# Kernel tuning notes

Hardware: AMD Instinct MI355X
Metric: run time of the kernel (lower is better)

Reference implementation:

```python
import jax, jax.numpy as jnp
import numpy as np

H = 12          # num_heads
T = 8           # num_temp_tokens (frames per video clip)


def _conv1d(z, w, b):
    # z: (Bv, C, T), w: (C_out, C_in, 3), padding=1, stride=1 (matches nn.Conv1d)
    y = jax.lax.conv_general_dilated(z, w, window_strides=(1,), padding=[(1, 1)],
                                     dimension_numbers=('NCH', 'OIH', 'NCH'))
    return y + b[None, :, None]


def setup_inputs() -> dict:
    key = jax.random.key(0)
    ks = jax.random.split(key, 9)
    B, N, C = 64, 197, 768
    s = 0.02
    return {
        'x': jax.random.normal(ks[0], (B, N, C), jnp.float32),
        'w_qkv': jax.random.normal(ks[1], (3 * C, C), jnp.float32) * s,
        'b_qkv': jax.random.normal(ks[2], (3 * C,), jnp.float32) * s,
        'w_proj': jax.random.normal(ks[3], (C, C), jnp.float32) * s,
        'b_proj': jax.random.normal(ks[4], (C,), jnp.float32) * s,
        'conv_q_w': jax.random.normal(ks[5], (C, C, 3), jnp.float32) * s,
        'conv_q_b': jax.random.normal(ks[6], (C,), jnp.float32) * s,
        'conv_k_w': jax.random.normal(ks[7], (C, C, 3), jnp.float32) * s,
        'conv_k_b': jax.random.normal(ks[8], (C,), jnp.float32) * s,
    }


def reference(x, w_qkv, b_qkv, w_proj, b_proj, conv_q_w, conv_q_b, conv_k_w, conv_k_b):
    B, N, C = x.shape
    Dh = C // H
    scale = Dh ** -0.5

    # temporal context from the CLS token across frames of each clip
    g = x[:, 0, :].reshape(B // T, T, C).transpose(0, 2, 1)          # (Bv, C, T)
    tcq = _conv1d(g, conv_q_w, conv_q_b).transpose(0, 2, 1).reshape(B, H, 1, Dh)
    tck = _conv1d(g, conv_k_w, conv_k_b).transpose(0, 2, 1).reshape(B, H, 1, Dh)

    qkv = (x @ w_qkv.T + b_qkv).reshape(B, N, 3, H, Dh).transpose(2, 0, 3, 1, 4)
    q, k, v = qkv[0], qkv[1], qkv[2]                                  # (B, H, N, Dh)

    # bias-added attention: (q + tcq) (k + tck)^T
    scores = jnp.einsum('bhnd,bhmd->bhnm', q + tcq, k + tck) * scale  # (B, H, N, N)
    attn = jax.nn.softmax(scores, axis=-1)
    out = jnp.einsum('bhnm,bhmd->bhnd', attn, v)                      # (B, H, N, Dh)
    out = out.transpose(0, 2, 1, 3).reshape(B, N, C)
    return out @ w_proj.T + b_proj
```

## Files before the change

kernel.cpp:

```cpp
#include <hip/hip_runtime.h>
#include <hip/hip_bf16.h>
#include <stdint.h>

typedef __attribute__((ext_vector_type(8))) short s16x8;
typedef __attribute__((ext_vector_type(4))) float f32x4;

#define MFMA16(a, b, c) __builtin_amdgcn_mfma_f32_16x16x32_bf16((a), (b), (c), 0, 0, 0)
#define SBAR() __builtin_amdgcn_s_barrier()

__device__ __forceinline__ void gl_lds16(const void* g, void* l) {
  __builtin_amdgcn_global_load_lds(
      (__attribute__((address_space(1))) void*)(void*)g,
      (__attribute__((address_space(3))) void*)l,
      16, 0, 0);
}

__device__ __forceinline__ unsigned short f2bf(float f) {
  union { float f; uint32_t u; } c; c.f = f;
  return (unsigned short)((c.u + 0x7FFFu + ((c.u >> 16) & 1u)) >> 16);
}

__device__ __forceinline__ f32x4 max4(f32x4 a, f32x4 b) {
  f32x4 c;
  c[0] = fmaxf(a[0], b[0]); c[1] = fmaxf(a[1], b[1]);
  c[2] = fmaxf(a[2], b[2]); c[3] = fmaxf(a[3], b[3]);
  return c;
}

__device__ __forceinline__ void xcd_swz(int GX, int GY, int& bx, int& by) {
  int nwg = GX * GY;
  int lid = by * GX + bx;
  int q = nwg >> 3, rm = nwg & 7;
  int xcd = lid & 7, off = lid >> 3;
  int nid = (xcd < rm ? xcd * (q + 1) : rm * (q + 1) + (xcd - rm) * q) + off;
  bx = nid % GX;
  by = nid / GX;
}

__global__ __launch_bounds__(256) void cvt_conv(
    const float* __restrict__ x, unsigned short* __restrict__ x_bf, int na4,
    const float* __restrict__ wqkv, unsigned short* __restrict__ wqkv_bf, int nb4,
    const float* __restrict__ wproj, unsigned short* __restrict__ wproj_bf, int nc4,
    const float* __restrict__ cqw, const float* __restrict__ ckw,
    float* __restrict__ tcpq, float* __restrict__ tcpk) {
  const int tid = threadIdx.x;
  const int bid = blockIdx.x;
  if (bid < 768) {
    __shared__ float g[192][10];
    const int clip = bid / 96;
    const int rem = bid % 96;
    const int chunk = rem >> 2;
    const int part = rem & 3;
    const int ci0 = part * 192;
    for (int i = tid; i < 192 * 8; i += 256) {
      int tt = i / 192, ci = i % 192;
      g[ci][tt + 1] = x[(size_t)(clip * 8 + tt) * 151296 + ci0 + ci];
    }
    for (int i = tid; i < 192; i += 256) { g[i][0] = 0.f; g[i][9] = 0.f; }
    __syncthreads();
    const int co = chunk * 32 + (tid >> 3);
    const int t = tid & 7;
    float aq = 0.f, ak = 0.f;
    const float* wqp = cqw + (size_t)co * 2304 + ci0 * 3;
    const float* wkp = ckw + (size_t)co * 2304 + ci0 * 3;
    for (int ci = 0; ci < 192; ++ci) {
      float g0 = g[ci][t], g1 = g[ci][t + 1], g2 = g[ci][t + 2];
      aq += g0 * wqp[ci * 3 + 0] + g1 * wqp[ci * 3 + 1] + g2 * wqp[ci * 3 + 2];
      ak += g0 * wkp[ci * 3 + 0] + g1 * wkp[ci * 3 + 1] + g2 * wkp[ci * 3 + 2];
    }
    int b = clip * 8 + t;
    tcpq[part * 49152 + b * 768 + co] = aq;
    tcpk[part * 49152 + b * 768 + co] = ak;
    return;
  }
  int i = (bid - 768) * 256 + tid;
  const float* src; unsigned short* dst; int j;
  if (i < na4) { src = x; dst = x_bf; j = i; }
  else if (i < na4 + nb4) { src = wqkv; dst = wqkv_bf; j = i - na4; }
  else if (i < na4 + nb4 + nc4) { src = wproj; dst = wproj_bf; j = i - na4 - nb4; }
  else return;
  float4 v = ((const float4*)src)[j];
  ushort4 o;
  o.x = f2bf(v.x); o.y = f2bf(v.y); o.z = f2bf(v.z); o.w = f2bf(v.w);
  ((ushort4*)dst)[j] = o;
}

__global__ __launch_bounds__(1024, 4) void qkv_attn(
    const unsigned short* __restrict__ X,
    const unsigned short* __restrict__ Wq,
    const float* __restrict__ bias,
    const float* __restrict__ tcpq, const float* __restrict__ tcpk,
    unsigned short* __restrict__ O) {
  union __align__(16) Smem {
    struct {
      unsigned short Xs[3][208][64];
      unsigned short Ws[3][192][64];
    } st;
    struct {
      unsigned short Qs[208][72];
      unsigned short Ks[208][72];
      unsigned short VTs[64][232];
      unsigned short Ps[13][16][40];
    } at;
  };
  __shared__ Smem U;
  __shared__ float tcb[3][64];

  const int tid = threadIdx.x;
  const int w = tid >> 6, lane = tid & 63;
  int bx = blockIdx.x, by0 = 0;
  xcd_swz(gridDim.x, 1, bx, by0);
  const int b = bx / 12, h = bx % 12;

  if (tid < 192) {
    int sec = tid >> 6, d = tid & 63;
    float v = bias[sec * 768 + h * 64 + d];
    if (sec < 2) {
      const float* tp = (sec == 0) ? tcpq : tcpk;
      int idx = b * 768 + h * 64 + d;
#pragma unroll
      for (int p = 0; p < 4; ++p) v += tp[p * 49152 + idx];
    }
    tcb[sec][d] = v;
  }

  const int wm = w >> 2, wn = w & 3;
  const int r = lane & 15, gq = lane >> 4;
  const int lrow = lane >> 3;
  const int lsw = ((lane & 7) ^ (lrow & 7)) * 8;
  const int mfn = (wm == 3) ? 4 : 3;

  f32x4 acc[4][3] = {};
  const size_t xbase = (size_t)b * 197 * 768;

  const int swzk[2] = { ((0 + gq) ^ (r & 7)) * 16, ((4 + gq) ^ (r & 7)) * 16 };
  const int rowA = (wm * 48 + r) * 128;
  const int rowB = (wn * 48 + r) * 128;

  auto stage = [&](int buf, int kc) {
#pragma unroll
    for (int j = 0; j < 2; ++j) {
      int c = w + j * 16;
      if (c < 26) {
        int row = c * 8 + lrow;
        gl_lds16(X + xbase + (size_t)row * 768 + kc * 64 + lsw,
                 (char*)&U.st.Xs[buf][0][0] + c * 1024);
      }
    }
#pragma unroll
    for (int j = 0; j < 2; ++j) {
      int c = w + j * 16;
      if (c < 24) {
        int wrow = c * 8 + lrow;
        int sec = wrow >> 6;
        gl_lds16(Wq + (size_t)(sec * 768 + h * 64 + (wrow & 63)) * 768 + kc * 64 + lsw,
                 (char*)&U.st.Ws[buf][0][0] + c * 1024);
      }
    }
  };

#define WAIT_OWN()                                                 \
  do {                                                             \
    if (w < 8)       asm volatile("s_waitcnt vmcnt(4)" ::: "memory"); \
    else if (w < 10) asm volatile("s_waitcnt vmcnt(3)" ::: "memory"); \
    else             asm volatile("s_waitcnt vmcnt(2)" ::: "memory"); \
  } while (0)

  stage(0, 0);
  stage(1, 1);
  WAIT_OWN();
  SBAR();

#pragma unroll
  for (int kc = 0; kc < 12; ++kc) {
    if (kc + 2 < 12) stage((kc + 2) % 3, kc + 2);
    const char* xb = (const char*)&U.st.Xs[kc % 3][0][0] + rowA;
    const char* wb = (const char*)&U.st.Ws[kc % 3][0][0] + rowB;
    __builtin_amdgcn_s_setprio(1);
#pragma unroll
    for (int kk = 0; kk < 2; ++kk) {
      s16x8 bfrg[3];
#pragma unroll
      for (int nf = 0; nf < 3; ++nf)
        bfrg[nf] = *(const s16x8*)(wb + nf * 2048 + swzk[kk]);
#pragma unroll
      for (int mf = 0; mf < 4; ++mf) {
        if (mf < mfn) {
          s16x8 afr = *(const s16x8*)(xb + mf * 2048 + swzk[kk]);
#pragma unroll
          for (int nf = 0; nf < 3; ++nf) acc[mf][nf] = MFMA16(afr, bfrg[nf], acc[mf][nf]);
        }
      }
    }
    __builtin_amdgcn_s_setprio(0);
    if (kc < 10) {
      WAIT_OWN();
      SBAR();
    } else if (kc == 10) {
      asm volatile("s_waitcnt vmcnt(0)" ::: "memory");
      SBAR();
    }
  }
  __syncthreads();

  for (int i = tid; i < 64 * 35; i += 1024) {
    int d = i / 35, c = 197 + i % 35;
    U.at.VTs[d][c] = 0;
  }
#pragma unroll
  for (int mf = 0; mf < 4; ++mf) {
    if (mf < mfn) {
#pragma unroll
      for (int nf = 0; nf < 3; ++nf) {
        int ncol = wn * 48 + nf * 16 + r;
        int sec = ncol >> 6, d = ncol & 63;
        float bb = tcb[sec][d];
#pragma unroll
        for (int rr = 0; rr < 4; ++rr) {
          int mrow = wm * 48 + mf * 16 + gq * 4 + rr;
          unsigned short bv = f2bf(acc[mf][nf][rr] + bb);
          if (sec == 0)      U.at.Qs[mrow][d] = bv;
          else if (sec == 1) U.at.Ks[mrow][d] = bv;
          else if (mrow < 197) U.at.VTs[d][mrow] = bv;
        }
      }
    }
  }
  __syncthreads();

  const int g = gq;
  for (int qt = w; qt < 13; qt += 16) {
    const int q0 = qt * 16;
    int qrow = q0 + r; if (qrow > 196) qrow = 196;
    s16x8 aq0 = *(const s16x8*)&U.at.Qs[qrow][g * 8];
    s16x8 aq1 = *(const s16x8*)&U.at.Qs[qrow][32 + g * 8];

    f32x4 s[13];
    __builtin_amdgcn_s_setprio(1);
#pragma unroll
    for (int j = 0; j < 13; ++j) {
      f32x4 z = {};
      z = MFMA16(aq0, *(const s16x8*)&U.at.Ks[j * 16 + r][g * 8], z);
      z = MFMA16(aq1, *(const s16x8*)&U.at.Ks[j * 16 + r][32 + g * 8], z);
      s[j] = z;
    }
    __builtin_amdgcn_s_setprio(0);
    if (r >= 5) { s[12][0] = -1e30f; s[12][1] = -1e30f; s[12][2] = -1e30f; s[12][3] = -1e30f; }

    f32x4 mx = s[0];
#pragma unroll
    for (int j = 1; j < 13; ++j) mx = max4(mx, s[j]);
#pragma unroll
    for (int off = 1; off < 16; off <<= 1) {
      f32x4 o_;
      o_[0] = __shfl_xor(mx[0], off, 64); o_[1] = __shfl_xor(mx[1], off, 64);
      o_[2] = __shfl_xor(mx[2], off, 64); o_[3] = __shfl_xor(mx[3], off, 64);
      mx = max4(mx, o_);
    }
    const float cexp = 0.125f * 1.44269504088896f;
    f32x4 sum = {};
#pragma unroll
    for (int j = 0; j < 13; ++j) {
      f32x4 p;
      p[0] = exp2f((s[j][0] - mx[0]) * cexp); p[1] = exp2f((s[j][1] - mx[1]) * cexp);
      p[2] = exp2f((s[j][2] - mx[2]) * cexp); p[3] = exp2f((s[j][3] - mx[3]) * cexp);
      s[j] = p;
      sum += p;
    }
#pragma unroll
    for (int off = 1; off < 16; off <<= 1) {
      sum[0] += __shfl_xor(sum[0], off, 64); sum[1] += __shfl_xor(sum[1], off, 64);
      sum[2] += __shfl_xor(sum[2], off, 64); sum[3] += __shfl_xor(sum[3], off, 64);
    }

    f32x4 o4[4] = {};
    for (int ks = 0; ks < 7; ++ks) {
      int j0 = ks * 2;
#pragma unroll
      for (int jj = 0; jj < 2; ++jj) {
        int jt = j0 + jj;
        int colb = jj * 16 + r;
        if (jt < 13) {
          f32x4 p = s[jt < 13 ? jt : 0];
          U.at.Ps[w][g * 4 + 0][colb] = f2bf(p[0]);
          U.at.Ps[w][g * 4 + 1][colb] = f2bf(p[1]);
          U.at.Ps[w][g * 4 + 2][colb] = f2bf(p[2]);
          U.at.Ps[w][g * 4 + 3][colb] = f2bf(p[3]);
        } else {
          U.at.Ps[w][g * 4 + 0][colb] = 0; U.at.Ps[w][g * 4 + 1][colb] = 0;
          U.at.Ps[w][g * 4 + 2][colb] = 0; U.at.Ps[w][g * 4 + 3][colb] = 0;
        }
      }
      asm volatile("s_waitcnt lgkmcnt(0)" ::: "memory");
      s16x8 ap = *(const s16x8*)&U.at.Ps[w][r][g * 8];
      __builtin_amdgcn_s_setprio(1);
#pragma unroll
      for (int n = 0; n < 4; ++n)
        o4[n] = MFMA16(ap, *(const s16x8*)&U.at.VTs[n * 16 + r][ks * 32 + g * 8], o4[n]);
      __builtin_amdgcn_s_setprio(0);
    }

    f32x4 rinv;
    rinv[0] = 1.0f / sum[0]; rinv[1] = 1.0f / sum[1];
    rinv[2] = 1.0f / sum[2]; rinv[3] = 1.0f / sum[3];
#pragma unroll
    for (int n = 0; n < 4; ++n) {
#pragma unroll
      for (int rr = 0; rr < 4; ++rr) {
        int qr = q0 + g * 4 + rr;
        if (qr < 197)
          O[((size_t)(b * 197 + qr)) * 768 + h * 64 + n * 16 + r] = f2bf(o4[n][rr] * rinv[rr]);
      }
    }
  }
#undef WAIT_OWN
}

__global__ __launch_bounds__(1024, 4) void proj_gemm(
    const unsigned short* __restrict__ A,
    const unsigned short* __restrict__ Bw,
    const float* __restrict__ bias,
    float* __restrict__ Out) {
  __shared__ __align__(16) unsigned short Xs[3][208][64];
  __shared__ __align__(16) unsigned short Ws[3][192][64];
  const int tid = threadIdx.x;
  const int w = tid >> 6, lane = tid & 63;
  int bx = blockIdx.x, by0 = 0;
  xcd_swz(gridDim.x, 1, bx, by0);
  const int b = bx >> 2, nt = bx & 3;
  const int wm = w >> 2, wn = w & 3;
  const int r = lane & 15, gq = lane >> 4;
  const int lrow = lane >> 3;
  const int lsw = ((lane & 7) ^ (lrow & 7)) * 8;
  const int mfn = (wm == 3) ? 4 : 3;

  f32x4 acc[4][3] = {};
  const size_t abase = (size_t)b * 197 * 768;
  const int swzk[2] = { ((0 + gq) ^ (r & 7)) * 16, ((4 + gq) ^ (r & 7)) * 16 };
  const int rowA = (wm * 48 + r) * 128;
  const int rowB = (wn * 48 + r) * 128;

  auto stage = [&](int buf, int kc) {
#pragma unroll
    for (int j = 0; j < 2; ++j) {
      int c = w + j * 16;
      if (c < 26) {
        int row = c * 8 + lrow;
        gl_lds16(A + abase + (size_t)row * 768 + kc * 64 + lsw,
                 (char*)&Xs[buf][0][0] + c * 1024);
      }
    }
#pragma unroll
    for (int j = 0; j < 2; ++j) {
      int c = w + j * 16;
      if (c < 24) {
        int wrow = c * 8 + lrow;
        gl_lds16(Bw + (size_t)(nt * 192 + wrow) * 768 + kc * 64 + lsw,
                 (char*)&Ws[buf][0][0] + c * 1024);
      }
    }
  };

#define WAIT_OWN()                                                 \
  do {                                                             \
    if (w < 8)       asm volatile("s_waitcnt vmcnt(4)" ::: "memory"); \
    else if (w < 10) asm volatile("s_waitcnt vmcnt(3)" ::: "memory"); \
    else             asm volatile("s_waitcnt vmcnt(2)" ::: "memory"); \
  } while (0)

  stage(0, 0);
  stage(1, 1);
  WAIT_OWN();
  SBAR();

#pragma unroll
  for (int kc = 0; kc < 12; ++kc) {
    if (kc + 2 < 12) stage((kc + 2) % 3, kc + 2);
    const char* xb = (const char*)&Xs[kc % 3][0][0] + rowA;
    const char* wb = (const char*)&Ws[kc % 3][0][0] + rowB;
    __builtin_amdgcn_s_setprio(1);
#pragma unroll
    for (int kk = 0; kk < 2; ++kk) {
      s16x8 bfrg[3];
#pragma unroll
      for (int nf = 0; nf < 3; ++nf)
        bfrg[nf] = *(const s16x8*)(wb + nf * 2048 + swzk[kk]);
#pragma unroll
      for (int mf = 0; mf < 4; ++mf) {
        if (mf < mfn) {
          s16x8 afr = *(const s16x8*)(xb + mf * 2048 + swzk[kk]);
#pragma unroll
          for (int nf = 0; nf < 3; ++nf) acc[mf][nf] = MFMA16(afr, bfrg[nf], acc[mf][nf]);
        }
      }
    }
    __builtin_amdgcn_s_setprio(0);
    if (kc < 10) {
      WAIT_OWN();
      SBAR();
    } else if (kc == 10) {
      asm volatile("s_waitcnt vmcnt(0)" ::: "memory");
      SBAR();
    }
  }

#pragma unroll
  for (int mf = 0; mf < 4; ++mf) {
    if (mf < mfn) {
#pragma unroll
      for (int nf = 0; nf < 3; ++nf) {
        int N = nt * 192 + wn * 48 + nf * 16 + r;
        float bb = bias[N];
#pragma unroll
        for (int rr = 0; rr < 4; ++rr) {
          int mrow = wm * 48 + mf * 16 + gq * 4 + rr;
          if (mrow < 197)
            Out[((size_t)(b * 197 + mrow)) * 768 + N] = acc[mf][nf][rr] + bb;
        }
      }
    }
  }
#undef WAIT_OWN
}

extern "C" void kernel_launch(void* const* d_in, const int* in_sizes, int n_in,
                              void* d_out, int out_size, void* d_ws, size_t ws_size,
                              hipStream_t stream) {
  const float* x       = (const float*)d_in[0];
  const float* w_qkv   = (const float*)d_in[1];
  const float* b_qkv   = (const float*)d_in[2];
  const float* w_proj  = (const float*)d_in[3];
  const float* b_proj  = (const float*)d_in[4];
  const float* conv_qw = (const float*)d_in[5];
  const float* conv_qb = (const float*)d_in[6];
  const float* conv_kw = (const float*)d_in[7];
  const float* conv_kb = (const float*)d_in[8];
  float* out = (float*)d_out;

  char* ws = (char*)d_ws;
  size_t off = 0;
  auto alloc = [&](size_t n) {
    char* p = ws + off;
    off = (off + n + 255) & ~(size_t)255;
    return p;
  };
  unsigned short* x_bf    = (unsigned short*)alloc(12608ull * 768 * 2);
  unsigned short* ao_bf   = (unsigned short*)alloc(12608ull * 768 * 2);
  unsigned short* wqkv_bf = (unsigned short*)alloc(2304ull * 768 * 2);
  unsigned short* wproj_bf= (unsigned short*)alloc(768ull * 768 * 2);
  float* tcpq = (float*)alloc(4ull * 64 * 768 * 4);
  float* tcpk = (float*)alloc(4ull * 64 * 768 * 4);
  if (off > ws_size) return;

  float* bias_comb = (float*)alloc(2304ull * 4);
  {
  }

  const int na4 = 2420736, nb4 = 442368, nc4 = 147456;
  const int cvt_blocks = (na4 + nb4 + nc4 + 255) / 256;
  cvt_conv<<<dim3(768 + cvt_blocks), 256, 0, stream>>>(
      x, x_bf, na4, w_qkv, wqkv_bf, nb4, w_proj, wproj_bf, nc4,
      conv_qw, conv_kw, tcpq, tcpk);
  {
    struct L {
      static __global__ void k(const float* bq, const float* cq, const float* ck,
                               float* o) {
        int i = blockIdx.x * 256 + threadIdx.x;
        if (i >= 2304) return;
        float v = bq[i];
        if (i < 768) v += cq[i];
        else if (i < 1536) v += ck[i - 768];
        o[i] = v;
      }
    };
    L::k<<<dim3(9), 256, 0, stream>>>(b_qkv, conv_qb, conv_kb, bias_comb);
  }
  qkv_attn<<<dim3(768), 1024, 0, stream>>>(x_bf, wqkv_bf, bias_comb, tcpq, tcpk, ao_bf);
  proj_gemm<<<dim3(256), 1024, 0, stream>>>(ao_bf, wproj_bf, b_proj, out);
}
```

Baseline: 152.7 us.

## Warp-specialize GEMM mainloops into producer and consumer waves; fold bias kernel into cvt

Both the fused QKV+attention kernel and the projection GEMM now use warp specialization. Waves 8-15 only issue global-to-LDS loads, and waves 0-7 only run MFMAs, each covering 112 rows × 48 columns with larger accumulator tiles. This aims to separate memory issue from compute and cut per-wave wait overhead, at the cost of half the waves doing no math and more accumulator registers per compute wave. The small bias-combining kernel is merged into the conversion kernel as one extra block, which saves a launch.

Result: slower. 285.5 us (+87.0%).

```diff
diff --git a/kernel.cpp b/kernel.cpp
--- a/kernel.cpp
+++ b/kernel.cpp
@@ -42,7 +42,9 @@
     const float* __restrict__ wqkv, unsigned short* __restrict__ wqkv_bf, int nb4,
     const float* __restrict__ wproj, unsigned short* __restrict__ wproj_bf, int nc4,
     const float* __restrict__ cqw, const float* __restrict__ ckw,
-    float* __restrict__ tcpq, float* __restrict__ tcpk) {
+    float* __restrict__ tcpq, float* __restrict__ tcpk,
+    const float* __restrict__ bqkv, const float* __restrict__ cqb,
+    const float* __restrict__ ckb, float* __restrict__ bias_comb, int last_bid) {
   const int tid = threadIdx.x;
   const int bid = blockIdx.x;
   if (bid < 768) {
@@ -71,6 +73,15 @@
     int b = clip * 8 + t;
     tcpq[part * 49152 + b * 768 + co] = aq;
     tcpk[part * 49152 + b * 768 + co] = ak;
+    return;
+  }
+  if (bid == last_bid) {
+    for (int i = tid; i < 2304; i += 256) {
+      float v = bqkv[i];
+      if (i < 768) v += cqb[i];
+      else if (i < 1536) v += ckb[i - 768];
+      bias_comb[i] = v;
+    }
     return;
   }
   int i = (bid - 768) * 256 + tid;
@@ -124,23 +135,24 @@
     tcb[sec][d] = v;
   }
 
-  const int wm = w >> 2, wn = w & 3;
   const int r = lane & 15, gq = lane >> 4;
   const int lrow = lane >> 3;
   const int lsw = ((lane & 7) ^ (lrow & 7)) * 8;
-  const int mfn = (wm == 3) ? 4 : 3;
-
-  f32x4 acc[4][3] = {};
+
+  const int wm = (w >> 2) & 1, wn = w & 3;
+  const int mfn = (wm == 0) ? 7 : 6;
+  const int swzk[2] = { ((0 + gq) ^ (r & 7)) * 16, ((4 + gq) ^ (r & 7)) * 16 };
+  const int rowA = (wm * 112 + r) * 128;
+  const int rowB = (wn * 48 + r) * 128;
+
+  f32x4 acc[7][3] = {};
   const size_t xbase = (size_t)b * 197 * 768;
 
-  const int swzk[2] = { ((0 + gq) ^ (r & 7)) * 16, ((4 + gq) ^ (r & 7)) * 16 };
-  const int rowA = (wm * 48 + r) * 128;
-  const int rowB = (wn * 48 + r) * 128;
-
+  const int pw = w - 8;
   auto stage = [&](int buf, int kc) {
 #pragma unroll
-    for (int j = 0; j < 2; ++j) {
-      int c = w + j * 16;
+    for (int j = 0; j < 4; ++j) {
+      int c = pw + j * 8;
       if (c < 26) {
         int row = c * 8 + lrow;
         gl_lds16(X + xbase + (size_t)row * 768 + kc * 64 + lsw,
@@ -148,58 +160,56 @@
       }
     }
 #pragma unroll
-    for (int j = 0; j < 2; ++j) {
-      int c = w + j * 16;
-      if (c < 24) {
-        int wrow = c * 8 + lrow;
-        int sec = wrow >> 6;
-        gl_lds16(Wq + (size_t)(sec * 768 + h * 64 + (wrow & 63)) * 768 + kc * 64 + lsw,
-                 (char*)&U.st.Ws[buf][0][0] + c * 1024);
-      }
+    for (int j = 0; j < 3; ++j) {
+      int c = pw + j * 8;
+      int wrow = c * 8 + lrow;
+      int sec = wrow >> 6;
+      gl_lds16(Wq + (size_t)(sec * 768 + h * 64 + (wrow & 63)) * 768 + kc * 64 + lsw,
+               (char*)&U.st.Ws[buf][0][0] + c * 1024);
     }
   };
 
-#define WAIT_OWN()                                                 \
-  do {                                                             \
-    if (w < 8)       asm volatile("s_waitcnt vmcnt(4)" ::: "memory"); \
-    else if (w < 10) asm volatile("s_waitcnt vmcnt(3)" ::: "memory"); \
-    else             asm volatile("s_waitcnt vmcnt(2)" ::: "memory"); \
+#define WAIT_P()                                                      \
+  do {                                                                \
+    if (w < 10) asm volatile("s_waitcnt vmcnt(7)" ::: "memory");      \
+    else        asm volatile("s_waitcnt vmcnt(6)" ::: "memory");      \
   } while (0)
 
-  stage(0, 0);
-  stage(1, 1);
-  WAIT_OWN();
+  if (w >= 8) {
+    stage(0, 0);
+    stage(1, 1);
+    WAIT_P();
+  }
   SBAR();
 
 #pragma unroll
   for (int kc = 0; kc < 12; ++kc) {
-    if (kc + 2 < 12) stage((kc + 2) % 3, kc + 2);
-    const char* xb = (const char*)&U.st.Xs[kc % 3][0][0] + rowA;
-    const char* wb = (const char*)&U.st.Ws[kc % 3][0][0] + rowB;
-    __builtin_amdgcn_s_setprio(1);
-#pragma unroll
-    for (int kk = 0; kk < 2; ++kk) {
-      s16x8 bfrg[3];
-#pragma unroll
-      for (int nf = 0; nf < 3; ++nf)
-        bfrg[nf] = *(const s16x8*)(wb + nf * 2048 + swzk[kk]);
-#pragma unroll
-      for (int mf = 0; mf < 4; ++mf) {
-        if (mf < mfn) {
-          s16x8 afr = *(const s16x8*)(xb + mf * 2048 + swzk[kk]);
-#pragma unroll
-          for (int nf = 0; nf < 3; ++nf) acc[mf][nf] = MFMA16(afr, bfrg[nf], acc[mf][nf]);
+    if (w >= 8) {
+      if (kc + 2 < 12) stage((kc + 2) % 3, kc + 2);
+      if (kc < 10) WAIT_P();
+      else if (kc == 10) asm volatile("s_waitcnt vmcnt(0)" ::: "memory");
+    } else {
+      const char* xb = (const char*)&U.st.Xs[kc % 3][0][0] + rowA;
+      const char* wb = (const char*)&U.st.Ws[kc % 3][0][0] + rowB;
+      __builtin_amdgcn_s_setprio(1);
+#pragma unroll
+      for (int kk = 0; kk < 2; ++kk) {
+        s16x8 bfrg[3];
+#pragma unroll
+        for (int nf = 0; nf < 3; ++nf)
+          bfrg[nf] = *(const s16x8*)(wb + nf * 2048 + swzk[kk]);
+#pragma unroll
+        for (int mf = 0; mf < 7; ++mf) {
+          if (mf < mfn) {
+            s16x8 afr = *(const s16x8*)(xb + mf * 2048 + swzk[kk]);
+#pragma unroll
+            for (int nf = 0; nf < 3; ++nf) acc[mf][nf] = MFMA16(afr, bfrg[nf], acc[mf][nf]);
+          }
         }
       }
-    }
-    __builtin_amdgcn_s_setprio(0);
-    if (kc < 10) {
-      WAIT_OWN();
-      SBAR();
-    } else if (kc == 10) {
-      asm volatile("s_waitcnt vmcnt(0)" ::: "memory");
-      SBAR();
-    }
+      __builtin_amdgcn_s_setprio(0);
+    }
+    SBAR();
   }
   __syncthreads();
 
@@ -207,21 +217,23 @@
     int d = i / 35, c = 197 + i % 35;
     U.at.VTs[d][c] = 0;
   }
-#pragma unroll
-  for (int mf = 0; mf < 4; ++mf) {
-    if (mf < mfn) {
-#pragma unroll
-      for (int nf = 0; nf < 3; ++nf) {
-        int ncol = wn * 48 + nf * 16 + r;
-        int sec = ncol >> 6, d = ncol & 63;
-        float bb = tcb[sec][d];
-#pragma unroll
-        for (int rr = 0; rr < 4; ++rr) {
-          int mrow = wm * 48 + mf * 16 + gq * 4 + rr;
-          unsigned short bv = f2bf(acc[mf][nf][rr] + bb);
-          if (sec == 0)      U.at.Qs[mrow][d] = bv;
-          else if (sec == 1) U.at.Ks[mrow][d] = bv;
-          else if (mrow < 197) U.at.VTs[d][mrow] = bv;
+  if (w < 8) {
+#pragma unroll
+    for (int mf = 0; mf < 7; ++mf) {
+      if (mf < mfn) {
+#pragma unroll
+        for (int nf = 0; nf < 3; ++nf) {
+          int ncol = wn * 48 + nf * 16 + r;
+          int sec = ncol >> 6, d = ncol & 63;
+          float bb = tcb[sec][d];
+#pragma unroll
+          for (int rr = 0; rr < 4; ++rr) {
+            int mrow = wm * 112 + mf * 16 + gq * 4 + rr;
+            unsigned short bv = f2bf(acc[mf][nf][rr] + bb);
+            if (sec == 0)      U.at.Qs[mrow][d] = bv;
+            else if (sec == 1) U.at.Ks[mrow][d] = bv;
+            else if (mrow < 197) U.at.VTs[d][mrow] = bv;
+          }
         }
       }
     }
@@ -313,7 +325,7 @@
       }
     }
   }
-#undef WAIT_OWN
+#undef WAIT_P
 }
 
 __global__ __launch_bounds__(1024, 4) void proj_gemm(
@@ -328,22 +340,24 @@
   int bx = blockIdx.x, by0 = 0;
   xcd_swz(gridDim.x, 1, bx, by0);
   const int b = bx >> 2, nt = bx & 3;
-  const int wm = w >> 2, wn = w & 3;
   const int r = lane & 15, gq = lane >> 4;
   const int lrow = lane >> 3;
   const int lsw = ((lane & 7) ^ (lrow & 7)) * 8;
-  const int mfn = (wm == 3) ? 4 : 3;
-
-  f32x4 acc[4][3] = {};
+
+  const int wm = (w >> 2) & 1, wn = w & 3;
+  const int mfn = (wm == 0) ? 7 : 6;
+  const int swzk[2] = { ((0 + gq) ^ (r & 7)) * 16, ((4 + gq) ^ (r & 7)) * 16 };
+  const int rowA = (wm * 112 + r) * 128;
+  const int rowB = (wn * 48 + r) * 128;
+
+  f32x4 acc[7][3] = {};
   const size_t abase = (size_t)b * 197 * 768;
-  const int swzk[2] = { ((0 + gq) ^ (r & 7)) * 16, ((4 + gq) ^ (r & 7)) * 16 };
-  const int rowA = (wm * 48 + r) * 128;
-  const int rowB = (wn * 48 + r) * 128;
+  const int pw = w - 8;
 
   auto stage = [&](int buf, int kc) {
 #pragma unroll
-    for (int j = 0; j < 2; ++j) {
-      int c = w + j * 16;
+    for (int j = 0; j < 4; ++j) {
+      int c = pw + j * 8;
       if (c < 26) {
         int row = c * 8 + lrow;
         gl_lds16(A + abase + (size_t)row * 768 + kc * 64 + lsw,
@@ -351,76 +365,76 @@
       }
     }
 #pragma unroll
-    for (int j = 0; j < 2; ++j) {
-      int c = w + j * 16;
-      if (c < 24) {
-        int wrow = c * 8 + lrow;
-        gl_lds16(Bw + (size_t)(nt * 192 + wrow) * 768 + kc * 64 + lsw,
-                 (char*)&Ws[buf][0][0] + c * 1024);
-      }
+    for (int j = 0; j < 3; ++j) {
+      int c = pw + j * 8;
+      int wrow = c * 8 + lrow;
+      gl_lds16(Bw + (size_t)(nt * 192 + wrow) * 768 + kc * 64 + lsw,
+               (char*)&Ws[buf][0][0] + c * 1024);
     }
   };
 
-#define WAIT_OWN()                                                 \
-  do {                                                             \
-    if (w < 8)       asm volatile("s_waitcnt vmcnt(4)" ::: "memory"); \
-    else if (w < 10) asm volatile("s_waitcnt vmcnt(3)" ::: "memory"); \
-    else             asm volatile("s_waitcnt vmcnt(2)" ::: "memory"); \
+#define WAIT_P()                                                      \
+  do {                                                                \
+    if (w < 10) asm volatile("s_waitcnt vmcnt(7)" ::: "memory");      \
+    else        asm volatile("s_waitcnt vmcnt(6)" ::: "memory");      \
   } while (0)
 
-  stage(0, 0);
-  stage(1, 1);
-  WAIT_OWN();
+  if (w >= 8) {
+    stage(0, 0);
+    stage(1, 1);
+    WAIT_P();
+  }
   SBAR();
 
 #pragma unroll
   for (int kc = 0; kc < 12; ++kc) {
-    if (kc + 2 < 12) stage((kc + 2) % 3, kc + 2);
-    const char* xb = (const char*)&Xs[kc % 3][0][0] + rowA;
-    const char* wb = (const char*)&Ws[kc % 3][0][0] + rowB;
-    __builtin_amdgcn_s_setprio(1);
-#pragma unroll
-    for (int kk = 0; kk < 2; ++kk) {
-      s16x8 bfrg[3];
-#pragma unroll
-      for (int nf = 0; nf < 3; ++nf)
-        bfrg[nf] = *(const s16x8*)(wb + nf * 2048 + swzk[kk]);
-#pragma unroll
-      for (int mf = 0; mf < 4; ++mf) {
-        if (mf < mfn) {
-          s16x8 afr = *(const s16x8*)(xb + mf * 2048 + swzk[kk]);
-#pragma unroll
-          for (int nf = 0; nf < 3; ++nf) acc[mf][nf] = MFMA16(afr, bfrg[nf], acc[mf][nf]);
+    if (w >= 8) {
+      if (kc + 2 < 12) stage((kc + 2) % 3, kc + 2);
+      if (kc < 10) WAIT_P();
+      else if (kc == 10) asm volatile("s_waitcnt vmcnt(0)" ::: "memory");
+    } else {
+      const char* xb = (const char*)&Xs[kc % 3][0][0] + rowA;
+      const char* wb = (const char*)&Ws[kc % 3][0][0] + rowB;
+      __builtin_amdgcn_s_setprio(1);
+#pragma unroll
+      for (int kk = 0; kk < 2; ++kk) {
+        s16x8 bfrg[3];
+#pragma unroll
+        for (int nf = 0; nf < 3; ++nf)
+          bfrg[nf] = *(const s16x8*)(wb + nf * 2048 + swzk[kk]);
+#pragma unroll
+        for (int mf = 0; mf < 7; ++mf) {
+          if (mf < mfn) {
+            s16x8 afr = *(const s16x8*)(xb + mf * 2048 + swzk[kk]);
+#pragma unroll
+            for (int nf = 0; nf < 3; ++nf) acc[mf][nf] = MFMA16(afr, bfrg[nf], acc[mf][nf]);
+          }
         }
       }
-    }
-    __builtin_amdgcn_s_setprio(0);
-    if (kc < 10) {
-      WAIT_OWN();
-      SBAR();
-    } else if (kc == 10) {
-      asm volatile("s_waitcnt vmcnt(0)" ::: "memory");
-      SBAR();
-    }
-  }
-
-#pragma unroll
-  for (int mf = 0; mf < 4; ++mf) {
-    if (mf < mfn) {
-#pragma unroll
-      for (int nf = 0; nf < 3; ++nf) {
-        int N = nt * 192 + wn * 48 + nf * 16 + r;
-        float bb = bias[N];
-#pragma unroll
-        for (int rr = 0; rr < 4; ++rr) {
-          int mrow = wm * 48 + mf * 16 + gq * 4 + rr;
-          if (mrow < 197)
-            Out[((size_t)(b * 197 + mrow)) * 768 + N] = acc[mf][nf][rr] + bb;
+      __builtin_amdgcn_s_setprio(0);
+    }
+    SBAR();
+  }
+
+  if (w < 8) {
+#pragma unroll
+    for (int mf = 0; mf < 7; ++mf) {
+      if (mf < mfn) {
+#pragma unroll
+        for (int nf = 0; nf < 3; ++nf) {
+          int N = nt * 192 + wn * 48 + nf * 16 + r;
+          float bb = bias[N];
+#pragma unroll
+          for (int rr = 0; rr < 4; ++rr) {
+            int mrow = wm * 112 + mf * 16 + gq * 4 + rr;
+            if (mrow < 197)
+              Out[((size_t)(b * 197 + mrow)) * 768 + N] = acc[mf][nf][rr] + bb;
+          }
         }
       }
     }
   }
-#undef WAIT_OWN
+#undef WAIT_P
 }
 
 extern "C" void kernel_launch(void* const* d_in, const int* in_sizes, int n_in,
@@ -450,31 +464,16 @@
   unsigned short* wproj_bf= (unsigned short*)alloc(768ull * 768 * 2);
   float* tcpq = (float*)alloc(4ull * 64 * 768 * 4);
   float* tcpk = (float*)alloc(4ull * 64 * 768 * 4);
+  float* bias_comb = (float*)alloc(2304ull * 4);
   if (off > ws_size) return;
-
-  float* bias_comb = (float*)alloc(2304ull * 4);
-  {
-  }
 
   const int na4 = 2420736, nb4 = 442368, nc4 = 147456;
   const int cvt_blocks = (na4 + nb4 + nc4 + 255) / 256;
-  cvt_conv<<<dim3(768 + cvt_blocks), 256, 0, stream>>>(
+  const int last_bid = 768 + cvt_blocks;
+  cvt_conv<<<dim3(last_bid + 1), 256, 0, stream>>>(
       x, x_bf, na4, w_qkv, wqkv_bf, nb4, w_proj, wproj_bf, nc4,
-      conv_qw, conv_kw, tcpq, tcpk);
-  {
-    struct L {
-      static __global__ void k(const float* bq, const float* cq, const float* ck,
-                               float* o) {
-        int i = blockIdx.x * 256 + threadIdx.x;
-        if (i >= 2304) return;
-        float v = bq[i];
-        if (i < 768) v += cq[i];
-        else if (i < 1536) v += ck[i - 768];
-        o[i] = v;
-      }
-    };
-    L::k<<<dim3(9), 256, 0, stream>>>(b_qkv, conv_qb, conv_kb, bias_comb);
-  }
+      conv_qw, conv_kw, tcpq, tcpk,
+      b_qkv, conv_qb, conv_kb, bias_comb, last_bid);
   qkv_attn<<<dim3(768), 1024, 0, stream>>>(x_bf, wqkv_bf, bias_comb, tcpq, tcpk, ao_bf);
   proj_gemm<<<dim3(256), 1024, 0, stream>>>(ao_bf, wproj_bf, b_proj, out);
 }
```

## Warp-specialize QKV GEMM with dedicated producer waves and fold bias kernel into conversion

Applied to the files above, without the earlier changes.

The QKV projection loop inside the fused attention kernel is restructured so 4 waves only issue global-to-LDS loads and 12 waves only run MFMAs on a reshaped 80-row M tiling. Consumers no longer wait on their own loads, only on the shared barrier, which is meant to hide load latency behind compute. The small bias-combination kernel is merged into the conversion kernel as an extra block, removing one launch. The trade-off is fewer MFMA waves doing more work each, plus higher register pressure from the 5x3 accumulator tile.

New measurement: 159.8 us. +4.7%, slower.

```diff
diff --git a/kernel.cpp b/kernel.cpp
--- a/kernel.cpp
+++ b/kernel.cpp
@@ -42,7 +42,9 @@
     const float* __restrict__ wqkv, unsigned short* __restrict__ wqkv_bf, int nb4,
     const float* __restrict__ wproj, unsigned short* __restrict__ wproj_bf, int nc4,
     const float* __restrict__ cqw, const float* __restrict__ ckw,
-    float* __restrict__ tcpq, float* __restrict__ tcpk) {
+    float* __restrict__ tcpq, float* __restrict__ tcpk,
+    const float* __restrict__ bqkv, const float* __restrict__ cqb,
+    const float* __restrict__ ckb, float* __restrict__ bias_comb, int last_bid) {
   const int tid = threadIdx.x;
   const int bid = blockIdx.x;
   if (bid < 768) {
@@ -71,6 +73,15 @@
     int b = clip * 8 + t;
     tcpq[part * 49152 + b * 768 + co] = aq;
     tcpk[part * 49152 + b * 768 + co] = ak;
+    return;
+  }
+  if (bid == last_bid) {
+    for (int i = tid; i < 2304; i += 256) {
+      float v = bqkv[i];
+      if (i < 768) v += cqb[i];
+      else if (i < 1536) v += ckb[i - 768];
+      bias_comb[i] = v;
+    }
     return;
   }
   int i = (bid - 768) * 256 + tid;
@@ -124,23 +135,24 @@
     tcb[sec][d] = v;
   }
 
-  const int wm = w >> 2, wn = w & 3;
   const int r = lane & 15, gq = lane >> 4;
   const int lrow = lane >> 3;
   const int lsw = ((lane & 7) ^ (lrow & 7)) * 8;
-  const int mfn = (wm == 3) ? 4 : 3;
-
-  f32x4 acc[4][3] = {};
+
+  const int wm = w >> 2, wn = w & 3;
+  const int mfn = (wm == 2) ? 3 : 5;
+  const int swzk[2] = { ((0 + gq) ^ (r & 7)) * 16, ((4 + gq) ^ (r & 7)) * 16 };
+  const int rowA = (wm * 80 + r) * 128;
+  const int rowB = (wn * 48 + r) * 128;
+
+  f32x4 acc[5][3] = {};
   const size_t xbase = (size_t)b * 197 * 768;
 
-  const int swzk[2] = { ((0 + gq) ^ (r & 7)) * 16, ((4 + gq) ^ (r & 7)) * 16 };
-  const int rowA = (wm * 48 + r) * 128;
-  const int rowB = (wn * 48 + r) * 128;
-
+  const int pw = w - 12;
   auto stage = [&](int buf, int kc) {
 #pragma unroll
-    for (int j = 0; j < 2; ++j) {
-      int c = w + j * 16;
+    for (int j = 0; j < 7; ++j) {
+      int c = pw + j * 4;
       if (c < 26) {
         int row = c * 8 + lrow;
         gl_lds16(X + xbase + (size_t)row * 768 + kc * 64 + lsw,
@@ -148,58 +160,56 @@
       }
     }
 #pragma unroll
-    for (int j = 0; j < 2; ++j) {
-      int c = w + j * 16;
-      if (c < 24) {
-        int wrow = c * 8 + lrow;
-        int sec = wrow >> 6;
-        gl_lds16(Wq + (size_t)(sec * 768 + h * 64 + (wrow & 63)) * 768 + kc * 64 + lsw,
-                 (char*)&U.st.Ws[buf][0][0] + c * 1024);
-      }
+    for (int j = 0; j < 6; ++j) {
+      int c = pw + j * 4;
+      int wrow = c * 8 + lrow;
+      int sec = wrow >> 6;
+      gl_lds16(Wq + (size_t)(sec * 768 + h * 64 + (wrow & 63)) * 768 + kc * 64 + lsw,
+               (char*)&U.st.Ws[buf][0][0] + c * 1024);
     }
   };
 
-#define WAIT_OWN()                                                 \
-  do {                                                             \
-    if (w < 8)       asm volatile("s_waitcnt vmcnt(4)" ::: "memory"); \
-    else if (w < 10) asm volatile("s_waitcnt vmcnt(3)" ::: "memory"); \
-    else             asm volatile("s_waitcnt vmcnt(2)" ::: "memory"); \
+#define WAIT_P()                                                      \
+  do {                                                                \
+    if (pw < 2) asm volatile("s_waitcnt vmcnt(13)" ::: "memory");     \
+    else        asm volatile("s_waitcnt vmcnt(12)" ::: "memory");     \
   } while (0)
 
-  stage(0, 0);
-  stage(1, 1);
-  WAIT_OWN();
+  if (w >= 12) {
+    stage(0, 0);
+    stage(1, 1);
+    WAIT_P();
+  }
   SBAR();
 
 #pragma unroll
   for (int kc = 0; kc < 12; ++kc) {
-    if (kc + 2 < 12) stage((kc + 2) % 3, kc + 2);
-    const char* xb = (const char*)&U.st.Xs[kc % 3][0][0] + rowA;
-    const char* wb = (const char*)&U.st.Ws[kc % 3][0][0] + rowB;
-    __builtin_amdgcn_s_setprio(1);
-#pragma unroll
-    for (int kk = 0; kk < 2; ++kk) {
-      s16x8 bfrg[3];
-#pragma unroll
-      for (int nf = 0; nf < 3; ++nf)
-        bfrg[nf] = *(const s16x8*)(wb + nf * 2048 + swzk[kk]);
-#pragma unroll
-      for (int mf = 0; mf < 4; ++mf) {
-        if (mf < mfn) {
-          s16x8 afr = *(const s16x8*)(xb + mf * 2048 + swzk[kk]);
-#pragma unroll
-          for (int nf = 0; nf < 3; ++nf) acc[mf][nf] = MFMA16(afr, bfrg[nf], acc[mf][nf]);
+    if (w >= 12) {
+      if (kc + 2 < 12) stage((kc + 2) % 3, kc + 2);
+      if (kc < 10) WAIT_P();
+      else if (kc == 10) asm volatile("s_waitcnt vmcnt(0)" ::: "memory");
+    } else {
+      const char* xb = (const char*)&U.st.Xs[kc % 3][0][0] + rowA;
+      const char* wb = (const char*)&U.st.Ws[kc % 3][0][0] + rowB;
+      __builtin_amdgcn_s_setprio(1);
+#pragma unroll
+      for (int kk = 0; kk < 2; ++kk) {
+        s16x8 bfrg[3];
+#pragma unroll
+        for (int nf = 0; nf < 3; ++nf)
+          bfrg[nf] = *(const s16x8*)(wb + nf * 2048 + swzk[kk]);
+#pragma unroll
+        for (int mf = 0; mf < 5; ++mf) {
+          if (mf < mfn) {
+            s16x8 afr = *(const s16x8*)(xb + mf * 2048 + swzk[kk]);
+#pragma unroll
+            for (int nf = 0; nf < 3; ++nf) acc[mf][nf] = MFMA16(afr, bfrg[nf], acc[mf][nf]);
+          }
         }
       }
-    }
-    __builtin_amdgcn_s_setprio(0);
-    if (kc < 10) {
-      WAIT_OWN();
-      SBAR();
-    } else if (kc == 10) {
-      asm volatile("s_waitcnt vmcnt(0)" ::: "memory");
-      SBAR();
-    }
+      __builtin_amdgcn_s_setprio(0);
+    }
+    SBAR();
   }
   __syncthreads();
 
@@ -207,21 +217,23 @@
     int d = i / 35, c = 197 + i % 35;
     U.at.VTs[d][c] = 0;
   }
-#pragma unroll
-  for (int mf = 0; mf < 4; ++mf) {
-    if (mf < mfn) {
-#pragma unroll
-      for (int nf = 0; nf < 3; ++nf) {
-        int ncol = wn * 48 + nf * 16 + r;
-        int sec = ncol >> 6, d = ncol & 63;
-        float bb = tcb[sec][d];
-#pragma unroll
-        for (int rr = 0; rr < 4; ++rr) {
-          int mrow = wm * 48 + mf * 16 + gq * 4 + rr;
-          unsigned short bv = f2bf(acc[mf][nf][rr] + bb);
-          if (sec == 0)      U.at.Qs[mrow][d] = bv;
-          else if (sec == 1) U.at.Ks[mrow][d] = bv;
-          else if (mrow < 197) U.at.VTs[d][mrow] = bv;
+  if (w < 12) {
+#pragma unroll
+    for (int mf = 0; mf < 5; ++mf) {
+      if (mf < mfn) {
+#pragma unroll
+        for (int nf = 0; nf < 3; ++nf) {
+          int ncol = wn * 48 + nf * 16 + r;
+          int sec = ncol >> 6, d = ncol & 63;
+          float bb = tcb[sec][d];
+#pragma unroll
+          for (int rr = 0; rr < 4; ++rr) {
+            int mrow = wm * 80 + mf * 16 + gq * 4 + rr;
+            unsigned short bv = f2bf(acc[mf][nf][rr] + bb);
+            if (sec == 0)      U.at.Qs[mrow][d] = bv;
+            else if (sec == 1) U.at.Ks[mrow][d] = bv;
+            else if (mrow < 197) U.at.VTs[d][mrow] = bv;
+          }
         }
       }
     }
@@ -313,7 +325,7 @@
       }
     }
   }
-#undef WAIT_OWN
+#undef WAIT_P
 }
 
 __global__ __launch_bounds__(1024, 4) void proj_gemm(
@@ -450,31 +462,16 @@
   unsigned short* wproj_bf= (unsigned short*)alloc(768ull * 768 * 2);
   float* tcpq = (float*)alloc(4ull * 64 * 768 * 4);
   float* tcpk = (float*)alloc(4ull * 64 * 768 * 4);
+  float* bias_comb = (float*)alloc(2304ull * 4);
   if (off > ws_size) return;
-
-  float* bias_comb = (float*)alloc(2304ull * 4);
-  {
-  }
 
   const int na4 = 2420736, nb4 = 442368, nc4 = 147456;
   const int cvt_blocks = (na4 + nb4 + nc4 + 255) / 256;
-  cvt_conv<<<dim3(768 + cvt_blocks), 256, 0, stream>>>(
+  const int last_bid = 768 + cvt_blocks;
+  cvt_conv<<<dim3(last_bid + 1), 256, 0, stream>>>(
       x, x_bf, na4, w_qkv, wqkv_bf, nb4, w_proj, wproj_bf, nc4,
-      conv_qw, conv_kw, tcpq, tcpk);
-  {
-    struct L {
-      static __global__ void k(const float* bq, const float* cq, const float* ck,
-                               float* o) {
-        int i = blockIdx.x * 256 + threadIdx.x;
-        if (i >= 2304) return;
-        float v = bq[i];
-        if (i < 768) v += cq[i];
-        else if (i < 1536) v += ck[i - 768];
-        o[i] = v;
-      }
-    };
-    L::k<<<dim3(9), 256, 0, stream>>>(b_qkv, conv_qb, conv_kb, bias_comb);
-  }
+      conv_qw, conv_kw, tcpq, tcpk,
+      b_qkv, conv_qb, conv_kb, bias_comb, last_bid);
   qkv_attn<<<dim3(768), 1024, 0, stream>>>(x_bf, wqkv_bf, bias_comb, tcpq, tcpk, ao_bf);
   proj_gemm<<<dim3(256), 1024, 0, stream>>>(ao_bf, wproj_bf, b_proj, out);
 }
```
